# Kernel tuning notes

Measured on AMD Instinct MI355X. Metric: run time of the kernel, lower is better.

Reference implementation:

```python
import jax, jax.numpy as jnp
import numpy as np

N = 100000
E = 6400000
H = 64  # hidden_nf


def setup_inputs() -> dict:
    key = jax.random.key(0)
    ks = jax.random.split(key, 12)
    x = jax.random.normal(ks[0], (N, 3), dtype=jnp.float32)
    vel = jax.random.normal(ks[1], (N, 3), dtype=jnp.float32)
    vel_norm = jax.random.uniform(ks[2], (N, 1), dtype=jnp.float32)
    edge_index = jax.random.randint(ks[3], (2, E), 0, N, dtype=jnp.int32)
    # coord_mlp_vel: Linear(1,H) -> LeakyReLU(0.2) -> Linear(H,1)
    W1 = jax.random.normal(ks[4], (H, 1), dtype=jnp.float32) * (1.0 / np.sqrt(1))
    b1 = jnp.zeros((H,), dtype=jnp.float32)
    W2 = jax.random.normal(ks[5], (1, H), dtype=jnp.float32) * (1.0 / np.sqrt(H))
    b2 = jnp.zeros((1,), dtype=jnp.float32)
    # phi: Linear(1,H) -> LeakyReLU(0.2) -> Linear(H,1,bias=False, xavier gain=0.001) -> Tanh
    Wp1 = jax.random.normal(ks[6], (H, 1), dtype=jnp.float32) * (1.0 / np.sqrt(1))
    bp1 = jnp.zeros((H,), dtype=jnp.float32)
    Wp2 = jax.random.normal(ks[7], (1, H), dtype=jnp.float32) * 0.001
    return {"x": x, "vel_norm": vel_norm, "vel": vel, "edge_index": edge_index,
            "W1": W1, "b1": b1, "W2": W2, "b2": b2,
            "Wp1": Wp1, "bp1": bp1, "Wp2": Wp2}


def reference(x, vel_norm, vel, edge_index, W1, b1, W2, b2, Wp1, bp1, Wp2):
    row, col = edge_index[0], edge_index[1]
    # edge_model: gather endpoint positions, radial distance -> tiny MLP -> scaled diff
    x_diff = x[row] - x[col]                                   # [E, 3]
    radial = jnp.sqrt(jnp.sum(x_diff * x_diff, axis=1, keepdims=True))  # [E, 1]
    h = jax.nn.leaky_relu(radial @ Wp1.T + bp1, 0.2)           # [E, H]
    e_out = jnp.tanh(h @ Wp2.T)                                # [E, 1]
    m_ij = x_diff * e_out                                      # [E, 3]
    # node_model: unsorted_segment_mean over row
    agg_sum = jax.ops.segment_sum(m_ij, row, num_segments=x.shape[0])           # [N, 3]
    cnt = jax.ops.segment_sum(jnp.ones((m_ij.shape[0], 1), m_ij.dtype), row,
                              num_segments=x.shape[0])                           # [N, 1]
    x_out = x + agg_sum / jnp.maximum(cnt, 1.0)
    # velocity term: x + vel * coord_mlp_vel(vel_norm)
    hv = jax.nn.leaky_relu(vel_norm @ W1.T + b1, 0.2)          # [N, H]
    scale = hv @ W2.T + b2                                     # [N, 1]
    return x_out + vel * scale
```

## Files before the change

kernel.cpp:

```cpp
#include <hip/hip_runtime.h>
#include <hip/hip_fp16.h>
#include <math.h>

#define LEAKY 0.2f
#define HDIM 64
#define EPB 4096
#define TPB1 256
#define PERT (EPB / TPB1)
#define RANGE 1024
#define RSH 10
#define KMAX 128
#define NSUB 4
#define NPART 6
#define NSLICE (NSUB * NPART)
#define FS2 262144.0f
#define INVFS2 (1.0f / 262144.0f)
#define FBIAS 4194304


__device__ __forceinline__ float fast_tanh(float v) {
    float e = __builtin_amdgcn_exp2f(v * 2.88539008178f);
    return 1.0f - 2.0f * __builtin_amdgcn_rcpf(e + 1.0f);
}

__device__ __noinline__ float edge_eo_slow(float rad,
                                           const float* sW1, const float* sb1,
                                           const float* sW2) {
    float a = 0.f;
    #pragma unroll 1
    for (int k = 0; k < HDIM; k++) {
        float h = fmaf(rad, sW1[k], sb1[k]);
        h = (h > 0.f) ? h : LEAKY * h;
        a = fmaf(sW2[k], h, a);
    }
    return fast_tanh(a);
}

__global__ void repack_h_kernel(const float* __restrict__ x, uint2* __restrict__ xh, int N,
                                const float* __restrict__ Wp1, const float* __restrict__ bp1,
                                const float* __restrict__ Wp2, float* __restrict__ consts,
                                uint4* __restrict__ acc4, unsigned* __restrict__ cursor, int K) {
    int i = blockIdx.x * blockDim.x + threadIdx.x;
    if (i < N) {
        unsigned hx = __half_as_ushort(__float2half(x[3*i]));
        unsigned hy = __half_as_ushort(__float2half(x[3*i+1]));
        unsigned hz = __half_as_ushort(__float2half(x[3*i+2]));
        xh[i] = make_uint2((hy << 16) | hx, hz);
        acc4[i] = make_uint4(0u, 0u, 0u, 0u);
    }
    if (blockIdx.x == 0) {
        if (threadIdx.x < 64) {
            int k = threadIdx.x;
            float w1 = Wp1[k];
            float slope = (w1 >= 0.f) ? 1.f : LEAKY;
            float c = Wp2[k] * w1 * slope;
            float bnz = (bp1[k] != 0.f) ? 1.f : 0.f;
            #pragma unroll
            for (int off = 32; off > 0; off >>= 1) {
                c += __shfl_down(c, off, 64);
                bnz += __shfl_down(bnz, off, 64);
            }
            if (k == 0) { consts[0] = c; consts[1] = bnz; }
        }
        for (int k = threadIdx.x; k < NSUB * K; k += 256) cursor[k] = 0u;
    }
}

__device__ __noinline__ void overflow_edge(unsigned rec, unsigned b_, const uint2* __restrict__ xh,
                              float C, bool slow,
                              const float* __restrict__ Wp1, const float* __restrict__ bp1,
                              const float* __restrict__ Wp2, unsigned* __restrict__ acc4) {
    unsigned lid = rec >> 17, col = rec & 0x1FFFFu;
    unsigned row = b_ * RANGE + lid;
    uint2 ga = xh[row], gb = xh[col];
    float ax = __half2float(__ushort_as_half((unsigned short)(ga.x & 0xFFFF)));
    float ay = __half2float(__ushort_as_half((unsigned short)(ga.x >> 16)));
    float az = __half2float(__ushort_as_half((unsigned short)(ga.y & 0xFFFF)));
    float bx = __half2float(__ushort_as_half((unsigned short)(gb.x & 0xFFFF)));
    float by = __half2float(__ushort_as_half((unsigned short)(gb.x >> 16)));
    float bz = __half2float(__ushort_as_half((unsigned short)(gb.y & 0xFFFF)));
    float dx = ax - bx, dy = ay - by, dz = az - bz;
    float rad = sqrtf(dx*dx + dy*dy + dz*dz);
    float eo;
    if (!slow) {
        eo = fast_tanh(C * rad);
    } else {
        float a = 0.f;
        for (int k = 0; k < HDIM; k++) {
            float h = fmaf(rad, Wp1[k], bp1[k]);
            h = (h > 0.f) ? h : LEAKY * h;
            a = fmaf(Wp2[k], h, a);
        }
        eo = fast_tanh(a);
    }
    atomicAdd(&acc4[4*row + 0], (unsigned)__float2int_rn(dx * eo * FS2));
    atomicAdd(&acc4[4*row + 1], (unsigned)__float2int_rn(dy * eo * FS2));
    atomicAdd(&acc4[4*row + 2], (unsigned)__float2int_rn(dz * eo * FS2));
    atomicAdd(&acc4[4*row + 3], 1u);
}

__global__ __launch_bounds__(TPB1) void sort5_kernel(
        const int* __restrict__ ei,
        const uint2* __restrict__ xh,
        const float* __restrict__ Wp1, const float* __restrict__ bp1,
        const float* __restrict__ Wp2, const float* __restrict__ consts,
        unsigned* __restrict__ cursor, unsigned* __restrict__ acc4,
        unsigned* __restrict__ recs, int E, int K, unsigned csub) {
    __shared__ unsigned stage[EPB];
    __shared__ unsigned hist[KMAX];
    __shared__ unsigned scanv[KMAX + 1];
    __shared__ unsigned gstart[KMAX];
    const float C = consts[0];
    const bool slow = (consts[1] != 0.f);
    const unsigned sub = (unsigned)blockIdx.x & (NSUB - 1);
    for (int k = threadIdx.x; k < K; k += TPB1) hist[k] = 0;
    __syncthreads();

    const size_t base = (size_t)blockIdx.x * EPB;
    const unsigned t = threadIdx.x;
    unsigned rc[PERT];
    unsigned meta[PERT];
    if (base + EPB <= (size_t)E && (E & 3) == 0) {
        const int4* pr = (const int4*)(ei + base);
        const int4* pc = (const int4*)(ei + (size_t)E + base);
        #pragma unroll
        for (int q = 0; q < PERT / 4; q++) {
            int4 rv = pr[t + q * TPB1];
            int4 cv = pc[t + q * TPB1];
            rc[4*q+0] = (((unsigned)rv.x & (RANGE-1)) << 17) | (unsigned)cv.x;
            rc[4*q+1] = (((unsigned)rv.y & (RANGE-1)) << 17) | (unsigned)cv.y;
            rc[4*q+2] = (((unsigned)rv.z & (RANGE-1)) << 17) | (unsigned)cv.z;
            rc[4*q+3] = (((unsigned)rv.w & (RANGE-1)) << 17) | (unsigned)cv.w;
            unsigned b0 = (unsigned)rv.x >> RSH;
            unsigned b1 = (unsigned)rv.y >> RSH;
            unsigned b2 = (unsigned)rv.z >> RSH;
            unsigned b3 = (unsigned)rv.w >> RSH;
            meta[4*q+0] = (b0 << 12) | atomicAdd(&hist[b0], 1u);
            meta[4*q+1] = (b1 << 12) | atomicAdd(&hist[b1], 1u);
            meta[4*q+2] = (b2 << 12) | atomicAdd(&hist[b2], 1u);
            meta[4*q+3] = (b3 << 12) | atomicAdd(&hist[b3], 1u);
        }
    } else {
        #pragma unroll
        for (int i = 0; i < PERT; i++) {
            size_t e = base + (size_t)i * TPB1 + t;
            meta[i] = 0xFFFFFFFFu;
            if (e < (size_t)E) {
                unsigned r = (unsigned)ei[e];
                unsigned c = (unsigned)ei[(size_t)E + e];
                rc[i] = ((r & (RANGE-1)) << 17) | c;
                unsigned b_ = r >> RSH;
                meta[i] = (b_ << 12) | atomicAdd(&hist[b_], 1u);
            }
        }
    }
    __syncthreads();
    unsigned res = 0;
    if (t < (unsigned)K) {
        unsigned myc = hist[t];
        if (myc) res = atomicAdd(&cursor[t * NSUB + sub], myc);
    }
    if (t >= 192) {
        int l = t - 192;
        unsigned origA = (l < K) ? hist[l] : 0u;
        unsigned origB = (l + 64 < K) ? hist[l + 64] : 0u;
        unsigned a = origA, b = origB;
        #pragma unroll
        for (int off = 1; off < 64; off <<= 1) {
            unsigned va = __shfl_up(a, off, 64);
            unsigned vb = __shfl_up(b, off, 64);
            if (l >= off) { a += va; b += vb; }
        }
        unsigned totA = __shfl(a, 63, 64);
        unsigned grand = totA + __shfl(b, 63, 64);
        scanv[l] = a - origA;
        scanv[l + 64] = totA + b - origB;
        if (l == 63) scanv[K] = grand;
    }
    __syncthreads();
    #pragma unroll
    for (int i = 0; i < PERT; i++) {
        if (meta[i] != 0xFFFFFFFFu) {
            unsigned bk_ = meta[i] >> 12;
            stage[scanv[bk_] + (meta[i] & 0xFFFu)] = rc[i];
        }
    }
    if (t < (unsigned)K) gstart[t] = res;
    __syncthreads();
    {
        const int wv = t >> 6, ln = (int)(t & 63u);
        for (int b_ = wv; b_ < K; b_ += 4) {
            unsigned lo = scanv[b_], hi = scanv[b_ + 1];
            unsigned gb = gstart[b_];
            unsigned* dst = recs + (size_t)(b_ * NSUB + sub) * csub;
            for (unsigned j = lo + ln; j < hi; j += 64) {
                unsigned off = gb + (j - lo);
                if (off < csub) dst[off] = stage[j];
                else            overflow_edge(stage[j], (unsigned)b_, xh, C, slow,
                                              Wp1, bp1, Wp2, acc4);
            }
        }
    }
}

__global__ __launch_bounds__(256, 4) void reduce8_kernel(
        const unsigned* __restrict__ recs, const unsigned* __restrict__ cursor,
        const uint2* __restrict__ xh,
        const float* __restrict__ Wp1, const float* __restrict__ bp1,
        const float* __restrict__ Wp2, const float* __restrict__ consts,
        uint4* __restrict__ slices, int N, int K, unsigned csub) {
    __shared__ unsigned long long accA[RANGE];
    __shared__ unsigned long long accB[RANGE];
    __shared__ float sW1[HDIM], sb1[HDIM], sW2[HDIM];
    const int b = blockIdx.x / NSLICE;
    const int s = blockIdx.x % NSLICE;
    const int r = s & (NSUB - 1);
    const int p = s >> 2;
    const float C = consts[0];
    const bool slow = (consts[1] != 0.f);
    const int nbase = b * RANGE;
    if (slow) {
        for (int k = threadIdx.x; k < HDIM; k += 256) {
            sW1[k] = Wp1[k]; sb1[k] = bp1[k]; sW2[k] = Wp2[k];
        }
    }
    for (int i = threadIdx.x; i < RANGE; i += 256) { accA[i] = 0ull; accB[i] = 0ull; }
    __syncthreads();
    unsigned cnt = cursor[b * NSUB + r];
    if (cnt > csub) cnt = csub;
    unsigned quads = (cnt + 3) >> 2;
    unsigned perq = (quads + NPART - 1) / NPART;
    unsigned q0 = (unsigned)p * perq;
    unsigned q1 = q0 + perq; if (q1 > quads) q1 = quads;
    const uint4* rb4 = (const uint4*)(recs + (size_t)(b * NSUB + r) * csub);

    #define PROC_REC(rec, idx)                                                     \
        if ((idx) < cnt) {                                                         \
            unsigned lid_ = (rec) >> 17, col_ = (rec) & 0x1FFFFu;                  \
            uint2 ga = xh[nbase + (int)lid_];                                      \
            uint2 gb = xh[col_];                                                   \
            float ax = __half2float(__ushort_as_half((unsigned short)(ga.x & 0xFFFF))); \
            float ay = __half2float(__ushort_as_half((unsigned short)(ga.x >> 16)));    \
            float az = __half2float(__ushort_as_half((unsigned short)(ga.y & 0xFFFF))); \
            float bx = __half2float(__ushort_as_half((unsigned short)(gb.x & 0xFFFF))); \
            float by = __half2float(__ushort_as_half((unsigned short)(gb.x >> 16)));    \
            float bz = __half2float(__ushort_as_half((unsigned short)(gb.y & 0xFFFF))); \
            float dx = ax - bx, dy = ay - by, dz = az - bz;                        \
            float rad = sqrtf(dx*dx + dy*dy + dz*dz);                              \
            float eo = slow ? edge_eo_slow(rad, sW1, sb1, sW2)                     \
                            : fast_tanh(C * rad);                                  \
            unsigned ix = (unsigned)(__float2int_rn(dx * eo * FS2) + FBIAS);       \
            unsigned iy = (unsigned)(__float2int_rn(dy * eo * FS2) + FBIAS);       \
            unsigned iz = (unsigned)(__float2int_rn(dz * eo * FS2) + FBIAS);       \
            atomicAdd(&accA[lid_], ((unsigned long long)ix << 32) | (unsigned long long)iy); \
            atomicAdd(&accB[lid_], ((unsigned long long)iz << 32) | 1ull);         \
        }

    unsigned q = q0 + threadIdx.x;
    while (q + 256 < q1) {
        uint4 v0 = rb4[q];
        uint4 v1 = rb4[q + 256];
        unsigned i0 = 4 * q, i1 = 4 * (q + 256);
        PROC_REC(v0.x, i0); PROC_REC(v0.y, i0 + 1);
        PROC_REC(v0.z, i0 + 2); PROC_REC(v0.w, i0 + 3);
        PROC_REC(v1.x, i1); PROC_REC(v1.y, i1 + 1);
        PROC_REC(v1.z, i1 + 2); PROC_REC(v1.w, i1 + 3);
        q += 512;
    }
    while (q < q1) {
        uint4 v = rb4[q];
        unsigned i0 = 4 * q;
        PROC_REC(v.x, i0); PROC_REC(v.y, i0 + 1);
        PROC_REC(v.z, i0 + 2); PROC_REC(v.w, i0 + 3);
        q += 256;
    }
    #undef PROC_REC
    __syncthreads();
    for (int i = threadIdx.x; i < RANGE; i += 256) {
        int node = nbase + i;
        if (node < N) {
            unsigned long long A = accA[i], B = accB[i];
            slices[(size_t)s * N + node] =
                make_uint4((unsigned)(A >> 32), (unsigned)A,
                           (unsigned)(B >> 32), (unsigned)B);
        }
    }
}

__global__ void node_merge_kernel(const float* __restrict__ x,
                                  const float* __restrict__ vel_norm,
                                  const float* __restrict__ vel,
                                  const float* __restrict__ W1, const float* __restrict__ b1,
                                  const float* __restrict__ W2, const float* __restrict__ b2,
                                  const uint4* __restrict__ slices,
                                  const uint4* __restrict__ acc4,
                                  float* __restrict__ out, int N) {
    __shared__ float sW1[HDIM], sb1[HDIM], sW2[HDIM];
    for (int k = threadIdx.x; k < HDIM; k += blockDim.x) {
        sW1[k] = W1[k]; sb1[k] = b1[k]; sW2[k] = W2[k];
    }
    __syncthreads();
    int i = blockIdx.x * blockDim.x + threadIdx.x;
    if (i >= N) return;
    unsigned long long sxb = 0, syb = 0, szb = 0;
    unsigned sc = 0;
    #pragma unroll
    for (int s = 0; s < NSLICE; s++) {
        uint4 v = slices[(size_t)s * N + i];
        sxb += v.x; syb += v.y; szb += v.z; sc += v.w;
    }
    uint4 a4 = acc4[i];
    long long fx = (long long)sxb - (long long)sc * (long long)FBIAS + (long long)(int)a4.x;
    long long fy = (long long)syb - (long long)sc * (long long)FBIAS + (long long)(int)a4.y;
    long long fz = (long long)szb - (long long)sc * (long long)FBIAS + (long long)(int)a4.z;
    float cntf = (float)(sc + a4.w);
    float sx = (float)fx * INVFS2;
    float sy = (float)fy * INVFS2;
    float sz = (float)fz * INVFS2;
    float vn = vel_norm[i];
    float a = b2[0];
    #pragma unroll
    for (int k = 0; k < HDIM; k++) {
        float h = fmaf(vn, sW1[k], sb1[k]);
        h = (h > 0.f) ? h : LEAKY * h;
        a = fmaf(sW2[k], h, a);
    }
    float inv = 1.0f / fmaxf(cntf, 1.0f);
    out[3*i]     = x[3*i]     + sx * inv + vel[3*i]     * a;
    out[3*i + 1] = x[3*i + 1] + sy * inv + vel[3*i + 1] * a;
    out[3*i + 2] = x[3*i + 2] + sz * inv + vel[3*i + 2] * a;
}

__global__ void precompute_kernel(const float* __restrict__ Wp1,
                                  const float* __restrict__ bp1,
                                  const float* __restrict__ Wp2,
                                  float* __restrict__ consts) {
    int k = threadIdx.x;
    float w1 = Wp1[k];
    float slope = (w1 >= 0.f) ? 1.f : LEAKY;
    float c = Wp2[k] * w1 * slope;
    float bnz = (bp1[k] != 0.f) ? 1.f : 0.f;
    #pragma unroll
    for (int off = 32; off > 0; off >>= 1) {
        c += __shfl_down(c, off, 64);
        bnz += __shfl_down(bnz, off, 64);
    }
    if (k == 0) { consts[0] = c; consts[1] = bnz; }
}

__global__ void edge_atomic_kernel(const float* __restrict__ x, const int* __restrict__ ei,
                                   const float* __restrict__ Wp1, const float* __restrict__ bp1,
                                   const float* __restrict__ Wp2, const float* __restrict__ consts,
                                   float* __restrict__ acc, int E) {
    __shared__ float sW1[HDIM], sb1[HDIM], sW2[HDIM];
    const float C = consts[0];
    const bool slow = (consts[1] != 0.f);
    if (slow) {
        for (int k = threadIdx.x; k < HDIM; k += blockDim.x) {
            sW1[k] = Wp1[k]; sb1[k] = bp1[k]; sW2[k] = Wp2[k];
        }
        __syncthreads();
    }
    int e = blockIdx.x * blockDim.x + threadIdx.x;
    if (e >= E) return;
    int r = ei[e];
    int c = ei[E + e];
    float dx = x[3*r] - x[3*c];
    float dy = x[3*r+1] - x[3*c+1];
    float dz = x[3*r+2] - x[3*c+2];
    float rad = sqrtf(dx*dx + dy*dy + dz*dz);
    float eo;
    if (!slow) {
        eo = fast_tanh(C * rad);
    } else {
        float a = 0.f;
        for (int k = 0; k < HDIM; k++) {
            float h = fmaf(rad, sW1[k], sb1[k]);
            h = (h > 0.f) ? h : LEAKY * h;
            a = fmaf(sW2[k], h, a);
        }
        eo = fast_tanh(a);
    }
    float* basep = acc + ((size_t)r << 2);
    atomicAdd(basep + 0, dx * eo);
    atomicAdd(basep + 1, dy * eo);
    atomicAdd(basep + 2, dz * eo);
    atomicAdd(basep + 3, 1.f);
}

__global__ void node_kernel(const float* __restrict__ x, const float* __restrict__ vel_norm,
                            const float* __restrict__ vel,
                            const float* __restrict__ W1, const float* __restrict__ b1,
                            const float* __restrict__ W2, const float* __restrict__ b2,
                            const float4* __restrict__ slices,
                            float* __restrict__ out, int N, int S) {
    __shared__ float sW1[HDIM], sb1[HDIM], sW2[HDIM];
    for (int k = threadIdx.x; k < HDIM; k += blockDim.x) {
        sW1[k] = W1[k]; sb1[k] = b1[k]; sW2[k] = W2[k];
    }
    __syncthreads();
    int i = blockIdx.x * blockDim.x + threadIdx.x;
    if (i >= N) return;
    float sx = 0.f, sy = 0.f, sz = 0.f, sc = 0.f;
    for (int s = 0; s < S; s++) {
        float4 v = slices[(size_t)s * N + i];
        sx += v.x; sy += v.y; sz += v.z; sc += v.w;
    }
    float vn = vel_norm[i];
    float a = b2[0];
    #pragma unroll
    for (int k = 0; k < HDIM; k++) {
        float h = fmaf(vn, sW1[k], sb1[k]);
        h = (h > 0.f) ? h : LEAKY * h;
        a = fmaf(sW2[k], h, a);
    }
    float inv = 1.0f / fmaxf(sc, 1.0f);
    out[3*i]     = x[3*i]     + sx * inv + vel[3*i]     * a;
    out[3*i + 1] = x[3*i + 1] + sy * inv + vel[3*i + 1] * a;
    out[3*i + 2] = x[3*i + 2] + sz * inv + vel[3*i + 2] * a;
}

extern "C" void kernel_launch(void* const* d_in, const int* in_sizes, int n_in,
                              void* d_out, int out_size, void* d_ws, size_t ws_size,
                              hipStream_t stream) {
    const float* x        = (const float*)d_in[0];
    const float* vel_norm = (const float*)d_in[1];
    const float* vel      = (const float*)d_in[2];
    const int*   ei       = (const int*)  d_in[3];
    const float* W1       = (const float*)d_in[4];
    const float* b1       = (const float*)d_in[5];
    const float* W2       = (const float*)d_in[6];
    const float* b2       = (const float*)d_in[7];
    const float* Wp1      = (const float*)d_in[8];
    const float* bp1      = (const float*)d_in[9];
    const float* Wp2      = (const float*)d_in[10];

    const int N = in_sizes[0] / 3;
    const int E = in_sizes[3] / 2;
    const int K = (N + RANGE - 1) / RANGE;
    const int nblk = (E + EPB - 1) / EPB;

    unsigned csub = (unsigned)(E / (K * NSUB)) + 1024u;
    csub = (csub + 63u) & ~63u;

    size_t rec_bytes = (size_t)K * NSUB * csub * sizeof(unsigned);
    size_t sp_slices = (rec_bytes + 15) & ~(size_t)15;
    size_t sp_xh     = sp_slices + (size_t)NSLICE * N * sizeof(uint4);
    size_t sp_acc    = (sp_xh + (size_t)N * sizeof(uint2) + 15) & ~(size_t)15;
    size_t sp_cur    = sp_acc + (size_t)N * sizeof(uint4);
    size_t sp_const  = (sp_cur + (size_t)NSUB * KMAX * sizeof(unsigned) + 15) & ~(size_t)15;
    size_t need      = sp_const + 32;

    if (K <= KMAX && ws_size >= need) {
        unsigned* recs   = (unsigned*)d_ws;
        uint4*    slices = (uint4*)   ((char*)d_ws + sp_slices);
        uint2*    xh     = (uint2*)   ((char*)d_ws + sp_xh);
        unsigned* acc4   = (unsigned*)((char*)d_ws + sp_acc);
        unsigned* cursor = (unsigned*)((char*)d_ws + sp_cur);
        float*    consts = (float*)   ((char*)d_ws + sp_const);

        repack_h_kernel<<<(N + 255) / 256, 256, 0, stream>>>(
            x, xh, N, Wp1, bp1, Wp2, consts, (uint4*)acc4, cursor, K);
        sort5_kernel<<<nblk, TPB1, 0, stream>>>(
            ei, xh, Wp1, bp1, Wp2, consts, cursor, acc4, recs, E, K, csub);
        reduce8_kernel<<<K * NSLICE, 256, 0, stream>>>(
            recs, cursor, xh, Wp1, bp1, Wp2, consts, slices, N, K, csub);
        node_merge_kernel<<<(N + 255) / 256, 256, 0, stream>>>(
            x, vel_norm, vel, W1, b1, W2, b2, slices, (const uint4*)acc4,
            (float*)d_out, N);
    } else {
        float* acc    = (float*)d_ws;
        float* consts = (float*)((char*)d_ws + (size_t)N * sizeof(float4));
        hipMemsetAsync(d_ws, 0, (size_t)N * sizeof(float4) + 32, stream);
        precompute_kernel<<<1, 64, 0, stream>>>(Wp1, bp1, Wp2, consts);
        edge_atomic_kernel<<<(E + 255) / 256, 256, 0, stream>>>(x, ei, Wp1, bp1, Wp2,
                                                                consts, acc, E);
        node_kernel<<<(N + 255) / 256, 256, 0, stream>>>(x, vel_norm, vel, W1, b1, W2, b2,
                                                         (const float4*)acc, (float*)d_out, N, 1);
    }
}
```

Before: 197.3 us.

## Flatten sort scatter loop, stage row positions in LDS, reduce partitions

The sort kernel now records each staged edge's bucket in shared memory and scatters all edges with one flat, thread-strided loop. This replaces the per-wave loop over buckets, which balanced work poorly across waves. The reduce kernel preloads the block's 1024 row-node positions into LDS instead of gathering them from global memory per edge, and reads records with nontemporal loads. NPART drops from 6 to 4, so fewer slices are written and merged, at the cost of fewer blocks and more work per block.

```diff
diff --git a/kernel.cpp b/kernel.cpp
--- a/kernel.cpp
+++ b/kernel.cpp
@@ -11,11 +11,13 @@
 #define RSH 10
 #define KMAX 128
 #define NSUB 4
-#define NPART 6
+#define NPART 4
 #define NSLICE (NSUB * NPART)
 #define FS2 262144.0f
 #define INVFS2 (1.0f / 262144.0f)
 #define FBIAS 4194304
+
+typedef unsigned int u32x4 __attribute__((ext_vector_type(4)));
 
 
 __device__ __forceinline__ float fast_tanh(float v) {
@@ -99,7 +101,7 @@
     atomicAdd(&acc4[4*row + 3], 1u);
 }
 
-__global__ __launch_bounds__(TPB1) void sort5_kernel(
+__global__ __launch_bounds__(TPB1) void sort6_kernel(
         const int* __restrict__ ei,
         const uint2* __restrict__ xh,
         const float* __restrict__ Wp1, const float* __restrict__ bp1,
@@ -107,6 +109,7 @@
         unsigned* __restrict__ cursor, unsigned* __restrict__ acc4,
         unsigned* __restrict__ recs, int E, int K, unsigned csub) {
     __shared__ unsigned stage[EPB];
+    __shared__ unsigned char bucket_of[EPB];
     __shared__ unsigned hist[KMAX];
     __shared__ unsigned scanv[KMAX + 1];
     __shared__ unsigned gstart[KMAX];
@@ -182,28 +185,24 @@
     for (int i = 0; i < PERT; i++) {
         if (meta[i] != 0xFFFFFFFFu) {
             unsigned bk_ = meta[i] >> 12;
-            stage[scanv[bk_] + (meta[i] & 0xFFFu)] = rc[i];
+            unsigned slot = scanv[bk_] + (meta[i] & 0xFFFu);
+            stage[slot] = rc[i];
+            bucket_of[slot] = (unsigned char)bk_;
         }
     }
     if (t < (unsigned)K) gstart[t] = res;
     __syncthreads();
-    {
-        const int wv = t >> 6, ln = (int)(t & 63u);
-        for (int b_ = wv; b_ < K; b_ += 4) {
-            unsigned lo = scanv[b_], hi = scanv[b_ + 1];
-            unsigned gb = gstart[b_];
-            unsigned* dst = recs + (size_t)(b_ * NSUB + sub) * csub;
-            for (unsigned j = lo + ln; j < hi; j += 64) {
-                unsigned off = gb + (j - lo);
-                if (off < csub) dst[off] = stage[j];
-                else            overflow_edge(stage[j], (unsigned)b_, xh, C, slow,
-                                              Wp1, bp1, Wp2, acc4);
-            }
-        }
-    }
-}
-
-__global__ __launch_bounds__(256, 4) void reduce8_kernel(
+    unsigned total = scanv[K];
+    for (unsigned j = t; j < total; j += TPB1) {
+        unsigned b_ = bucket_of[j];
+        unsigned off = gstart[b_] + (j - scanv[b_]);
+        if (off < csub) recs[(size_t)(b_ * NSUB + sub) * csub + off] = stage[j];
+        else            overflow_edge(stage[j], (unsigned)b_, xh, C, slow,
+                                      Wp1, bp1, Wp2, acc4);
+    }
+}
+
+__global__ __launch_bounds__(256, 4) void reduce9_kernel(
         const unsigned* __restrict__ recs, const unsigned* __restrict__ cursor,
         const uint2* __restrict__ xh,
         const float* __restrict__ Wp1, const float* __restrict__ bp1,
@@ -211,6 +210,7 @@
         uint4* __restrict__ slices, int N, int K, unsigned csub) {
     __shared__ unsigned long long accA[RANGE];
     __shared__ unsigned long long accB[RANGE];
+    __shared__ uint2 sxh[RANGE];
     __shared__ float sW1[HDIM], sb1[HDIM], sW2[HDIM];
     const int b = blockIdx.x / NSLICE;
     const int s = blockIdx.x % NSLICE;
@@ -224,20 +224,24 @@
             sW1[k] = Wp1[k]; sb1[k] = bp1[k]; sW2[k] = Wp2[k];
         }
     }
-    for (int i = threadIdx.x; i < RANGE; i += 256) { accA[i] = 0ull; accB[i] = 0ull; }
+    for (int i = threadIdx.x; i < RANGE; i += 256) {
+        accA[i] = 0ull; accB[i] = 0ull;
+        int src = nbase + i;
+        sxh[i] = xh[(src < N) ? src : 0];
+    }
     __syncthreads();
     unsigned cnt = cursor[b * NSUB + r];
     if (cnt > csub) cnt = csub;
     unsigned quads = (cnt + 3) >> 2;
-    unsigned perq = (quads + NPART - 1) / NPART;
+    unsigned perq = (quads + 3) >> 2;
     unsigned q0 = (unsigned)p * perq;
     unsigned q1 = q0 + perq; if (q1 > quads) q1 = quads;
-    const uint4* rb4 = (const uint4*)(recs + (size_t)(b * NSUB + r) * csub);
+    const u32x4* rb4 = (const u32x4*)(recs + (size_t)(b * NSUB + r) * csub);
 
     #define PROC_REC(rec, idx)                                                     \
         if ((idx) < cnt) {                                                         \
             unsigned lid_ = (rec) >> 17, col_ = (rec) & 0x1FFFFu;                  \
-            uint2 ga = xh[nbase + (int)lid_];                                      \
+            uint2 ga = sxh[lid_];                                                  \
             uint2 gb = xh[col_];                                                   \
             float ax = __half2float(__ushort_as_half((unsigned short)(ga.x & 0xFFFF))); \
             float ay = __half2float(__ushort_as_half((unsigned short)(ga.x >> 16)));    \
@@ -258,8 +262,8 @@
 
     unsigned q = q0 + threadIdx.x;
     while (q + 256 < q1) {
-        uint4 v0 = rb4[q];
-        uint4 v1 = rb4[q + 256];
+        u32x4 v0 = __builtin_nontemporal_load(&rb4[q]);
+        u32x4 v1 = __builtin_nontemporal_load(&rb4[q + 256]);
         unsigned i0 = 4 * q, i1 = 4 * (q + 256);
         PROC_REC(v0.x, i0); PROC_REC(v0.y, i0 + 1);
         PROC_REC(v0.z, i0 + 2); PROC_REC(v0.w, i0 + 3);
@@ -268,7 +272,7 @@
         q += 512;
     }
     while (q < q1) {
-        uint4 v = rb4[q];
+        u32x4 v = __builtin_nontemporal_load(&rb4[q]);
         unsigned i0 = 4 * q;
         PROC_REC(v.x, i0); PROC_REC(v.y, i0 + 1);
         PROC_REC(v.z, i0 + 2); PROC_REC(v.w, i0 + 3);
@@ -461,9 +465,9 @@
 
         repack_h_kernel<<<(N + 255) / 256, 256, 0, stream>>>(
             x, xh, N, Wp1, bp1, Wp2, consts, (uint4*)acc4, cursor, K);
-        sort5_kernel<<<nblk, TPB1, 0, stream>>>(
+        sort6_kernel<<<nblk, TPB1, 0, stream>>>(
             ei, xh, Wp1, bp1, Wp2, consts, cursor, acc4, recs, E, K, csub);
-        reduce8_kernel<<<K * NSLICE, 256, 0, stream>>>(
+        reduce9_kernel<<<K * NSLICE, 256, 0, stream>>>(
             recs, cursor, xh, Wp1, bp1, Wp2, consts, slices, N, K, csub);
         node_merge_kernel<<<(N + 255) / 256, 256, 0, stream>>>(
             x, vel_norm, vel, W1, b1, W2, b2, slices, (const uint4*)acc4,
```

Result: faster. 186.9 us (-5.3%).
